# Optimization experiments

Measured on AMD Instinct MI355X. Metric: run time of the kernel, lower is better.

## Reference

```python
import jax, jax.numpy as jnp
import numpy as np

N, Q, D = 512, 1024, 256  # num_nodes(=batch), query_len(context len), input_dim


def setup_inputs() -> dict:
    key = jax.random.key(0)
    ks = jax.random.split(key, 7)
    return {
        "query": jax.random.normal(ks[0], (N, 1, D), dtype=jnp.float32),
        "context": jax.random.normal(ks[1], (N, Q, D), dtype=jnp.float32),
        # torch nn.Linear weights are [out_features, in_features]
        "W_in": jax.random.normal(ks[2], (D, D), dtype=jnp.float32) / np.sqrt(D).astype(np.float32),
        "W_out": jax.random.normal(ks[3], (D, 2 * D), dtype=jnp.float32) / np.sqrt(2 * D).astype(np.float32),
        # per-node decay params [num_nodes,1,1]; positive so exp(-ab*dt) decays
        "ae": jax.random.uniform(ks[4], (N, 1, 1), dtype=jnp.float32),
        "ad": jax.random.uniform(ks[5], (N, 1, 1), dtype=jnp.float32),
        "ab": jax.random.uniform(ks[6], (N, 1, 1), dtype=jnp.float32),
        "index": 0,  # stored on self in the original, unused in forward math
    }


def reference(query, context, W_in, W_out, ae, ad, ab, index):
    # general attention: project query
    q = query @ W_in.T                                   # [N,1,D]
    scores = jnp.einsum('bod,bqd->boq', q, context)      # [N,1,Q]
    attention_weights = jax.nn.softmax(scores, axis=-1)  # [N,1,Q]
    ctx_t = jnp.swapaxes(context, 1, 2)                  # [N,D,Q]
    mix = attention_weights * ctx_t                      # [N,D,Q]  (broadcast over D)
    # delta_t = flip(arange(Q)) = [Q-1, ..., 0]
    delta_t = jnp.arange(Q - 1, -1, -1, dtype=jnp.float32)[None, None, :]  # [1,1,Q]
    bt = jnp.exp(-ab * delta_t)                          # [N,1,Q]
    mb = mix * bt                                        # [N,D,Q]
    term_2 = jnp.abs(ae * mb)
    term_3 = jnp.abs(ad * mb)  # |-ad * mix * bt| == |ad * mix * bt|
    mix2 = jnp.tanh(jnp.sum(term_2 + mix - term_3, axis=-1))[:, None, :]  # [N,1,D]
    combined = jnp.concatenate([mix2, q], axis=2)        # [N,1,2D]
    output = jnp.tanh(combined @ W_out.T)                # [N,1,D]
    return output, attention_weights
```

## Files before the change

kernel.cpp:

```cpp
#include <hip/hip_runtime.h>
#include <math.h>

#define N_NODES 512
#define QLEN    1024
#define DIM     256
#define TJ      16
#define LROW    264
#define NT      (QLEN / TJ)
#define NBUF    3

#define AS1 __attribute__((address_space(1)))
#define AS3 __attribute__((address_space(3)))
#define GLD16(gsrc, ldst) \
  __builtin_amdgcn_global_load_lds((AS1 const void*)(gsrc), (AS3 void*)(ldst), 16, 0, 0)

__global__ __launch_bounds__(256, 2) void rpps_fused_kernel(
    const float* __restrict__ query,
    const float* __restrict__ context,
    const float* __restrict__ W_in,
    const float* __restrict__ W_out,
    const float* __restrict__ ae,
    const float* __restrict__ ad,
    const float* __restrict__ ab,
    float* __restrict__ out,
    float* __restrict__ scores_out)
{
  __shared__ float qs[DIM];
  __shared__ float qv[DIM];
  __shared__ float sc[QLEN];
  __shared__ float comb[2 * DIM];
  __shared__ float redM[4], redL[4];
  __shared__ float redA[4][DIM], redB[4][DIM];
  __shared__ float tile[NBUF][TJ * LROW];

  const int b    = blockIdx.x;
  const int tid  = threadIdx.x;
  const int wave = tid >> 6;
  const int lane = tid & 63;
  const int wg   = (tid >> 4) & 3;
  const int gl   = tid & 15;
  const int row  = 4 * wave + wg;

  const float* ctx = context + (size_t)b * QLEN * DIM;

  qs[tid] = query[b * DIM + tid];

  #pragma unroll
  for (int i = 0; i < 4; ++i)
    GLD16(ctx + (size_t)(4 * wave + i) * DIM + lane * 4,
          &tile[0][(4 * wave + i) * LROW]);
  #pragma unroll
  for (int i = 0; i < 4; ++i)
    GLD16(ctx + (size_t)(TJ + 4 * wave + i) * DIM + lane * 4,
          &tile[1][(4 * wave + i) * LROW]);

  asm volatile("s_waitcnt lgkmcnt(0)\n\ts_barrier" ::: "memory");

  float qp = 0.f;
  {
    const float4* w4 = (const float4*)(W_in + (size_t)tid * DIM);
    #pragma unroll 8
    for (int k = 0; k < DIM / 4; ++k) {
      const float4 wv = w4[k];
      qp += wv.x * qs[4 * k] + wv.y * qs[4 * k + 1] +
            wv.z * qs[4 * k + 2] + wv.w * qs[4 * k + 3];
    }
  }
  qv[tid] = qp;
  asm volatile("s_waitcnt lgkmcnt(0)\n\ts_barrier" ::: "memory");

  float qreg[16];
  #pragma unroll
  for (int k = 0; k < 16; ++k) qreg[k] = qv[gl + 16 * k];

  const float ab_v = ab[b];
  float m_w = -INFINITY, l_w = 0.f;
  float accA[16], accB[16];
  #pragma unroll
  for (int k = 0; k < 16; ++k) { accA[k] = 0.f; accB[k] = 0.f; }

  int slot_c = 0, slot_p = 2;
  for (int t = 0; t < NT; ++t) {
    if (t < NT - 1) asm volatile("s_waitcnt vmcnt(4)" ::: "memory");
    else            asm volatile("s_waitcnt vmcnt(0)" ::: "memory");

    if (t + 2 < NT) {
      const float* src = ctx + (size_t)(t + 2) * TJ * DIM;
      float* dst = &tile[slot_p][0];
      #pragma unroll
      for (int i = 0; i < 4; ++i)
        GLD16(src + (size_t)(4 * wave + i) * DIM + lane * 4,
              dst + (4 * wave + i) * LROW);
    }

    const float* trow = &tile[slot_c][row * LROW + gl];
    float c[16];
    #pragma unroll
    for (int k = 0; k < 16; ++k) c[k] = trow[16 * k];

    float s = 0.f;
    #pragma unroll
    for (int k = 0; k < 16; ++k) s += c[k] * qreg[k];
    s += __shfl_xor(s, 1);
    s += __shfl_xor(s, 2);
    s += __shfl_xor(s, 4);
    s += __shfl_xor(s, 8);

    if (gl == 0) sc[t * TJ + row] = s;

    float tm = fmaxf(s, __shfl_xor(s, 16));
    tm = fmaxf(tm, __shfl_xor(tm, 32));

    if (tm > m_w) {
      const float rsc = __expf(m_w - tm);
      m_w = tm;
      l_w *= rsc;
      #pragma unroll
      for (int k = 0; k < 16; ++k) { accA[k] *= rsc; accB[k] *= rsc; }
    }

    const float w  = __expf(s - m_w);
    const float bt = __expf(-ab_v * (float)(QLEN - 1 - (t * TJ + row)));
    const float wb = w * bt;
    l_w += w;
    #pragma unroll
    for (int k = 0; k < 16; ++k) {
      accA[k] += w * c[k];
      accB[k] += wb * fabsf(c[k]);
    }

    if (++slot_c == NBUF) slot_c = 0;
    if (++slot_p == NBUF) slot_p = 0;
  }

  #pragma unroll
  for (int k = 0; k < 16; ++k) {
    accA[k] += __shfl_xor(accA[k], 16);
    accA[k] += __shfl_xor(accA[k], 32);
    accB[k] += __shfl_xor(accB[k], 16);
    accB[k] += __shfl_xor(accB[k], 32);
  }
  l_w += __shfl_xor(l_w, 16);
  l_w += __shfl_xor(l_w, 32);

  if (lane == 0) { redM[wave] = m_w; redL[wave] = l_w; }
  if (wg == 0) {
    #pragma unroll
    for (int k = 0; k < 16; ++k) {
      redA[wave][gl + 16 * k] = accA[k];
      redB[wave][gl + 16 * k] = accB[k];
    }
  }
  __syncthreads();

  const float M  = fmaxf(fmaxf(redM[0], redM[1]), fmaxf(redM[2], redM[3]));
  const float e0 = __expf(redM[0] - M), e1 = __expf(redM[1] - M);
  const float e2 = __expf(redM[2] - M), e3 = __expf(redM[3] - M);
  const float L  = e0 * redL[0] + e1 * redL[1] + e2 * redL[2] + e3 * redL[3];
  const float A  = e0 * redA[0][tid] + e1 * redA[1][tid] +
                   e2 * redA[2][tid] + e3 * redA[3][tid];
  const float B  = e0 * redB[0][tid] + e1 * redB[1][tid] +
                   e2 * redB[2][tid] + e3 * redB[3][tid];
  const float invL = 1.f / L;
  const float cb   = fabsf(ae[b]) - fabsf(ad[b]);

  comb[tid]       = tanhf((A + cb * B) * invL);
  comb[DIM + tid] = qp;

  #pragma unroll
  for (int c2 = 0; c2 < 4; ++c2) {
    const int j = c2 * 256 + tid;
    scores_out[(size_t)b * QLEN + j] = __expf(sc[j] - M) * invL;
  }

  __syncthreads();

  float oacc = 0.f;
  {
    const float4* wo4 = (const float4*)(W_out + (size_t)tid * 2 * DIM);
    #pragma unroll 8
    for (int k = 0; k < (2 * DIM) / 4; ++k) {
      const float4 wv = wo4[k];
      oacc += wv.x * comb[4 * k] + wv.y * comb[4 * k + 1] +
              wv.z * comb[4 * k + 2] + wv.w * comb[4 * k + 3];
    }
  }
  out[(size_t)b * DIM + tid] = tanhf(oacc);
}

extern "C" void kernel_launch(void* const* d_in, const int* in_sizes, int n_in,
                              void* d_out, int out_size, void* d_ws, size_t ws_size,
                              hipStream_t stream) {
  const float* query   = (const float*)d_in[0];
  const float* context = (const float*)d_in[1];
  const float* W_in    = (const float*)d_in[2];
  const float* W_out   = (const float*)d_in[3];
  const float* ae      = (const float*)d_in[4];
  const float* ad      = (const float*)d_in[5];
  const float* ab      = (const float*)d_in[6];

  float* out        = (float*)d_out;
  float* scores_out = (float*)d_out + N_NODES * DIM;

  hipLaunchKernelGGL(rpps_fused_kernel, dim3(N_NODES), dim3(256), 0, stream,
                     query, context, W_in, W_out, ae, ad, ab, out, scores_out);
}
```

Baseline: 724.8 us.

## Split context sequence across two blocks per node with a separate merge kernel

Each node's 1024-row context is now split into two halves handled by separate blocks, doubling the grid to 1024 blocks, and each block writes its partial softmax state (max, sum, accumulators) to workspace. A second kernel merges the partials, computes the output projection and normalizes the scores. The per-block pipeline drops from three buffers to two with a different wait pattern, and the launch bound asks for 4 blocks per CU, so more blocks can be resident to hide memory latency. This costs a second launch, extra workspace traffic for the partials, and the W_in projection being computed twice per node.

```diff
diff --git a/kernel.cpp b/kernel.cpp
--- a/kernel.cpp
+++ b/kernel.cpp
@@ -6,34 +6,34 @@
 #define DIM     256
 #define TJ      16
 #define LROW    264
-#define NT      (QLEN / TJ)
-#define NBUF    3
+#define HROWS   512
+#define NT      (HROWS / TJ)
 
 #define AS1 __attribute__((address_space(1)))
 #define AS3 __attribute__((address_space(3)))
 #define GLD16(gsrc, ldst) \
   __builtin_amdgcn_global_load_lds((AS1 const void*)(gsrc), (AS3 void*)(ldst), 16, 0, 0)
 
-__global__ __launch_bounds__(256, 2) void rpps_fused_kernel(
+__global__ __launch_bounds__(256, 4) void rpps_half_kernel(
     const float* __restrict__ query,
     const float* __restrict__ context,
     const float* __restrict__ W_in,
-    const float* __restrict__ W_out,
-    const float* __restrict__ ae,
-    const float* __restrict__ ad,
     const float* __restrict__ ab,
-    float* __restrict__ out,
-    float* __restrict__ scores_out)
+    float* __restrict__ scores_raw,
+    float* __restrict__ Wm,
+    float* __restrict__ Wl,
+    float* __restrict__ WA,
+    float* __restrict__ WB,
+    float* __restrict__ Wq)
 {
   __shared__ float qs[DIM];
   __shared__ float qv[DIM];
-  __shared__ float sc[QLEN];
-  __shared__ float comb[2 * DIM];
-  __shared__ float redM[4], redL[4];
-  __shared__ float redA[4][DIM], redB[4][DIM];
-  __shared__ float tile[NBUF][TJ * LROW];
-
-  const int b    = blockIdx.x;
+  __shared__ float sc[HROWS];
+  __shared__ float tile[2][TJ * LROW];
+
+  const int bid  = blockIdx.x;
+  const int b    = bid >> 1;
+  const int h    = bid & 1;
   const int tid  = threadIdx.x;
   const int wave = tid >> 6;
   const int lane = tid & 63;
@@ -41,7 +41,7 @@
   const int gl   = tid & 15;
   const int row  = 4 * wave + wg;
 
-  const float* ctx = context + (size_t)b * QLEN * DIM;
+  const float* ctx = context + ((size_t)b * QLEN + (size_t)h * HROWS) * DIM;
 
   qs[tid] = query[b * DIM + tid];
 
@@ -49,10 +49,6 @@
   for (int i = 0; i < 4; ++i)
     GLD16(ctx + (size_t)(4 * wave + i) * DIM + lane * 4,
           &tile[0][(4 * wave + i) * LROW]);
-  #pragma unroll
-  for (int i = 0; i < 4; ++i)
-    GLD16(ctx + (size_t)(TJ + 4 * wave + i) * DIM + lane * 4,
-          &tile[1][(4 * wave + i) * LROW]);
 
   asm volatile("s_waitcnt lgkmcnt(0)\n\ts_barrier" ::: "memory");
 
@@ -79,21 +75,24 @@
   #pragma unroll
   for (int k = 0; k < 16; ++k) { accA[k] = 0.f; accB[k] = 0.f; }
 
-  int slot_c = 0, slot_p = 2;
   for (int t = 0; t < NT; ++t) {
-    if (t < NT - 1) asm volatile("s_waitcnt vmcnt(4)" ::: "memory");
-    else            asm volatile("s_waitcnt vmcnt(0)" ::: "memory");
-
-    if (t + 2 < NT) {
-      const float* src = ctx + (size_t)(t + 2) * TJ * DIM;
-      float* dst = &tile[slot_p][0];
+    const int cur = t & 1;
+
+    asm volatile("s_waitcnt lgkmcnt(0)" ::: "memory");
+
+    if (t + 1 < NT) {
+      const float* src = ctx + (size_t)(t + 1) * TJ * DIM;
+      float* dst = &tile[cur ^ 1][0];
       #pragma unroll
       for (int i = 0; i < 4; ++i)
         GLD16(src + (size_t)(4 * wave + i) * DIM + lane * 4,
               dst + (4 * wave + i) * LROW);
-    }
-
-    const float* trow = &tile[slot_c][row * LROW + gl];
+      asm volatile("s_waitcnt vmcnt(4)" ::: "memory");
+    } else {
+      asm volatile("s_waitcnt vmcnt(0)" ::: "memory");
+    }
+
+    const float* trow = &tile[cur][row * LROW + gl];
     float c[16];
     #pragma unroll
     for (int k = 0; k < 16; ++k) c[k] = trow[16 * k];
@@ -120,7 +119,7 @@
     }
 
     const float w  = __expf(s - m_w);
-    const float bt = __expf(-ab_v * (float)(QLEN - 1 - (t * TJ + row)));
+    const float bt = __expf(-ab_v * (float)(QLEN - 1 - (h * HROWS + t * TJ + row)));
     const float wb = w * bt;
     l_w += w;
     #pragma unroll
@@ -128,9 +127,6 @@
       accA[k] += w * c[k];
       accB[k] += wb * fabsf(c[k]);
     }
-
-    if (++slot_c == NBUF) slot_c = 0;
-    if (++slot_p == NBUF) slot_p = 0;
   }
 
   #pragma unroll
@@ -143,36 +139,60 @@
   l_w += __shfl_xor(l_w, 16);
   l_w += __shfl_xor(l_w, 32);
 
-  if (lane == 0) { redM[wave] = m_w; redL[wave] = l_w; }
+  const int widx = ((b * 2 + h) << 2) + wave;
+  if (lane == 0) { Wm[widx] = m_w; Wl[widx] = l_w; }
   if (wg == 0) {
     #pragma unroll
     for (int k = 0; k < 16; ++k) {
-      redA[wave][gl + 16 * k] = accA[k];
-      redB[wave][gl + 16 * k] = accB[k];
-    }
-  }
+      WA[(size_t)widx * DIM + gl + 16 * k] = accA[k];
+      WB[(size_t)widx * DIM + gl + 16 * k] = accB[k];
+    }
+  }
+  if (h == 0) Wq[b * DIM + tid] = qp;
+
   __syncthreads();
-
-  const float M  = fmaxf(fmaxf(redM[0], redM[1]), fmaxf(redM[2], redM[3]));
-  const float e0 = __expf(redM[0] - M), e1 = __expf(redM[1] - M);
-  const float e2 = __expf(redM[2] - M), e3 = __expf(redM[3] - M);
-  const float L  = e0 * redL[0] + e1 * redL[1] + e2 * redL[2] + e3 * redL[3];
-  const float A  = e0 * redA[0][tid] + e1 * redA[1][tid] +
-                   e2 * redA[2][tid] + e3 * redA[3][tid];
-  const float B  = e0 * redB[0][tid] + e1 * redB[1][tid] +
-                   e2 * redB[2][tid] + e3 * redB[3][tid];
+  #pragma unroll
+  for (int c2 = 0; c2 < 2; ++c2) {
+    const int j = c2 * 256 + tid;
+    scores_raw[(size_t)b * QLEN + h * HROWS + j] = sc[j];
+  }
+}
+
+__global__ __launch_bounds__(256) void rpps_merge_kernel(
+    const float* __restrict__ W_out,
+    const float* __restrict__ ae,
+    const float* __restrict__ ad,
+    const float* __restrict__ Wm,
+    const float* __restrict__ Wl,
+    const float* __restrict__ WA,
+    const float* __restrict__ WB,
+    const float* __restrict__ Wq,
+    float* __restrict__ out,
+    float* __restrict__ scores)
+{
+  __shared__ float comb[2 * DIM];
+  const int b = blockIdx.x, tid = threadIdx.x;
+
+  float mv[8];
+  #pragma unroll
+  for (int w = 0; w < 8; ++w) mv[w] = Wm[b * 8 + w];
+  float M = mv[0];
+  #pragma unroll
+  for (int w = 1; w < 8; ++w) M = fmaxf(M, mv[w]);
+
+  float L = 0.f, A = 0.f, B = 0.f;
+  #pragma unroll
+  for (int w = 0; w < 8; ++w) {
+    const float e = __expf(mv[w] - M);
+    L += e * Wl[b * 8 + w];
+    A += e * WA[(size_t)(b * 8 + w) * DIM + tid];
+    B += e * WB[(size_t)(b * 8 + w) * DIM + tid];
+  }
   const float invL = 1.f / L;
   const float cb   = fabsf(ae[b]) - fabsf(ad[b]);
 
   comb[tid]       = tanhf((A + cb * B) * invL);
-  comb[DIM + tid] = qp;
-
-  #pragma unroll
-  for (int c2 = 0; c2 < 4; ++c2) {
-    const int j = c2 * 256 + tid;
-    scores_out[(size_t)b * QLEN + j] = __expf(sc[j] - M) * invL;
-  }
-
+  comb[DIM + tid] = Wq[b * DIM + tid];
   __syncthreads();
 
   float oacc = 0.f;
@@ -186,6 +206,13 @@
     }
   }
   out[(size_t)b * DIM + tid] = tanhf(oacc);
+
+  #pragma unroll
+  for (int c2 = 0; c2 < 4; ++c2) {
+    const int j = c2 * 256 + tid;
+    const float s = scores[(size_t)b * QLEN + j];
+    scores[(size_t)b * QLEN + j] = __expf(s - M) * invL;
+  }
 }
 
 extern "C" void kernel_launch(void* const* d_in, const int* in_sizes, int n_in,
@@ -202,6 +229,14 @@
   float* out        = (float*)d_out;
   float* scores_out = (float*)d_out + N_NODES * DIM;
 
-  hipLaunchKernelGGL(rpps_fused_kernel, dim3(N_NODES), dim3(256), 0, stream,
-                     query, context, W_in, W_out, ae, ad, ab, out, scores_out);
+  float* Wm = (float*)d_ws;
+  float* Wl = Wm + N_NODES * 8;
+  float* WA = Wl + N_NODES * 8;
+  float* WB = WA + (size_t)N_NODES * 8 * DIM;
+  float* Wq = WB + (size_t)N_NODES * 8 * DIM;
+
+  hipLaunchKernelGGL(rpps_half_kernel, dim3(N_NODES * 2), dim3(256), 0, stream,
+                     query, context, W_in, ab, scores_out, Wm, Wl, WA, WB, Wq);
+  hipLaunchKernelGGL(rpps_merge_kernel, dim3(N_NODES), dim3(256), 0, stream,
+                     W_out, ae, ad, Wm, Wl, WA, WB, Wq, out, scores_out);
 }
```

New measurement: 747.0 us. +3.1%, slower.
